# Kernel optimization log

Measured on AMD Instinct MI355X. Metric: run time of the kernel, lower is better.

The kernel has to match this reference:

```python
import jax, jax.numpy as jnp
import numpy as np

B, S, D, E = 4, 1024, 1024, 4
HID = 2816  # multiple_of * ceil(int(2*4*D/3) / multiple_of), multiple_of=256
COND = 1024  # min(D, 1024)
NORM_EPS = 1e-5  # block norms
LN_EPS = 1e-5    # q_norm/k_norm default eps


def setup_inputs() -> dict:
    key = jax.random.key(0)
    ks = jax.random.split(key, 16)
    w = lambda i, shape: jax.random.normal(ks[i], shape, jnp.float32) * 0.02
    return {
        'x': jax.random.normal(ks[0], (B, S, D), jnp.float32),
        'freqs_cis': jax.random.normal(ks[1], (S, 32), jnp.float32),  # unused by the block
        'adaln_input': jax.random.normal(ks[2], (B, COND), jnp.float32),
        'wq': w(3, (D, D)), 'wk': w(4, (D, D)), 'wv': w(5, (D, D)), 'wo': w(6, (D, D)),
        'q_norm_w': jnp.ones((D,), jnp.float32), 'q_norm_b': jnp.zeros((D,), jnp.float32),
        'k_norm_w': jnp.ones((D,), jnp.float32), 'k_norm_b': jnp.zeros((D,), jnp.float32),
        'attn_norm_w': jnp.ones((D,), jnp.float32), 'attn_norm_b': jnp.zeros((D,), jnp.float32),
        'ffn_norm_w': jnp.ones((D,), jnp.float32), 'ffn_norm_b': jnp.zeros((D,), jnp.float32),
        'w1': w(7, (E, D, HID)), 'w2': w(8, (E, HID, D)), 'w3': w(9, (E, D, HID)),
        'router_w': w(10, (D, E)), 'router_b': jnp.zeros((E,), jnp.float32),
        'ada_w': w(11, (COND, 6 * D)), 'ada_b': jnp.zeros((6 * D,), jnp.float32),
    }


def _ln(x, w, b, eps):
    mu = jnp.mean(x, -1, keepdims=True)
    var = jnp.mean((x - mu) ** 2, -1, keepdims=True)
    return (x - mu) * jax.lax.rsqrt(var + eps) * w + b


def _attention(x, wq, wk, wv, wo, qn_w, qn_b, kn_w, kn_b):
    # NOTE: this module attends over the FEATURE dim (no head split, no 1/sqrt(d) scale):
    # xq,xk,xv are permuted to [B, D, S]; scores are [B, D, D].
    q = _ln(x @ wq, qn_w, qn_b, LN_EPS)
    k = _ln(x @ wk, kn_w, kn_b, LN_EPS)
    v = x @ wv
    scores = jnp.einsum('bsd,bse->bde', q, k)          # [B, D, D]
    attn = jax.nn.softmax(scores, axis=-1)
    out = jnp.einsum('bde,bse->bsd', attn, v)          # [B, S, D]
    return out @ wo


def _moe(x, w1, w2, w3, router_w, router_b):
    logits = x @ router_w + router_b                   # [B, S, E]
    # F.normalize default dim=1 -> L2-normalize along the SEQUENCE dim (faithful quirk)
    nrm = jnp.sqrt(jnp.sum(logits * logits, axis=1, keepdims=True))
    logits = logits / jnp.maximum(nrm, 1e-12)
    probs = jax.nn.softmax(logits, axis=-1)
    topw, topi = jax.lax.top_k(probs, 2)
    # dense combine weights [B,S,E]: identical math to the masked gather/scatter dispatch
    combine = jnp.sum(jax.nn.one_hot(topi, E, dtype=x.dtype) * topw[..., None], axis=-2)
    h1 = jnp.einsum('bsd,edh->ebsh', x, w1)
    h3 = jnp.einsum('bsd,edh->ebsh', x, w3)
    out_e = jnp.einsum('ebsh,ehd->ebsd', jnp.sin(h1) * h3, w2)
    moe = jnp.einsum('bse,ebsd->bsd', combine, out_e)
    avg = jnp.mean(probs, axis=0)                      # [S, E] (mean over batch dim only)
    aux = jnp.sum((1.0 / E - avg) ** 2)
    return moe, aux


def reference(x, freqs_cis, adaln_input, wq, wk, wv, wo, q_norm_w, q_norm_b, k_norm_w,
              k_norm_b, attn_norm_w, attn_norm_b, ffn_norm_w, ffn_norm_b, w1, w2, w3,
              router_w, router_b, ada_w, ada_b):
    ada = jax.nn.silu(adaln_input) @ ada_w + ada_b     # [B, 6D]
    shift_msa, scale_msa, gate_msa, shift_mlp, scale_mlp, gate_mlp = jnp.split(ada, 6, axis=1)
    h = _ln(x, attn_norm_w, attn_norm_b, NORM_EPS)
    h = h * (1.0 + scale_msa[:, None, :]) + shift_msa[:, None, :]
    x = x + gate_msa[:, None, :] * _attention(h, wq, wk, wv, wo, q_norm_w, q_norm_b, k_norm_w, k_norm_b)
    h = _ln(x, ffn_norm_w, ffn_norm_b, NORM_EPS)
    h = h * (1.0 + scale_mlp[:, None, :]) + shift_mlp[:, None, :]
    # MoE path REPLACES x (no residual, gate_mlp unused) — faithful to the source
    x, aux = _moe(h, w1, w2, w3, router_w, router_b)
    return x, aux
```

## Files before the change

### kernel.cpp

```cpp
#include <hip/hip_runtime.h>
#include <hip/hip_bf16.h>
#include <math.h>

#define BB 4
#define SS 1024
#define DD 1024
#define EE 4
#define HID 2816
#define HC 1408
#define SIXD 6144
#define NSLOT 8704
#define NMB 68

typedef __bf16 v8bf __attribute__((ext_vector_type(8)));
typedef float  v4f  __attribute__((ext_vector_type(4)));

__device__ __forceinline__ ushort f2bf(float f) {
    union { float f; unsigned u; } v; v.f = f;
    unsigned r = v.u + 0x7fff + ((v.u >> 16) & 1);
    return (ushort)(r >> 16);
}
__device__ __forceinline__ float bf2f(ushort u) {
    union { unsigned u; float f; } v; v.u = ((unsigned)u) << 16;
    return v.f;
}
__device__ __forceinline__ void split_bf(float x, ushort& h, ushort& l) {
    h = f2bf(x);
    l = f2bf(x - bf2f(h));
}
__device__ __forceinline__ void gload16(const void* g, void* l) {
    __builtin_amdgcn_global_load_lds((const __attribute__((address_space(1))) void*)g,
                                     (__attribute__((address_space(3))) void*)l, 16, 0, 0);
}
template<int N> __device__ __forceinline__ void wait_vm() {
    __builtin_amdgcn_s_waitcnt((N & 15) | (0x7 << 4) | (0xF << 8) | ((N >> 4) << 14));
}

__device__ __forceinline__ void xcd_remap(int& bx, int& by) {
    const int gx = gridDim.x, gy = gridDim.y;
    const int nwg = gx * gy;
    const int wid = bx + gx * by;
    const int q = nwg >> 3, r = nwg & 7;
    const int xcd = wid & 7, loc = wid >> 3;
    const int pos = (xcd < r) ? (xcd * (q + 1) + loc)
                              : (r * (q + 1) + (xcd - r) * q + loc);
    bx = pos % gx; by = pos / gx;
}

__device__ __forceinline__ void xcd_remap_cm(int& bx, int& by) {
    const int gx = gridDim.x, gy = gridDim.y;
    const int nwg = gx * gy;
    const int wid = bx + gx * by;
    const int q = nwg >> 3, r = nwg & 7;
    const int xcd = wid & 7, loc = wid >> 3;
    const int pos = (xcd < r) ? (xcd * (q + 1) + loc)
                              : (r * (q + 1) + (xcd - r) * q + loc);
    bx = pos / gy; by = pos % gy;
}

__device__ __forceinline__ void moe_remap(int& bx, int& by) {
    const int gx = gridDim.x, gy = gridDim.y;
    const int total = gx * gy;
    const int wid = bx + gx * by;
    if ((total & 7) || (gx & 1)) { xcd_remap(bx, by); return; }
    const int q = total >> 3;
    const int pos = (wid & 7) * q + (wid >> 3);
    const int NG = gx >> 1;
    const int gh = NG * gy;
    const int nh = pos / gh, r = pos % gh;
    by = r / NG;
    bx = nh * NG + (r % NG);
}

template<int EPI, bool SPLIT, bool MOE>
__global__ __launch_bounds__(256, 2) void mgemm(
    const ushort* __restrict__ Ah, const ushort* __restrict__ Al,
    const ushort* __restrict__ Bh, const ushort* __restrict__ Bl,
    void* __restrict__ Cv, ushort* __restrict__ C2,
    const float* __restrict__ f1, const float* __restrict__ f2,
    const int* __restrict__ tokidx, const int* __restrict__ mbe,
    const int* __restrict__ mbm,
    int K, int lda, int ldb, int ldc,
    long sA, long sB, long sC)
{
    constexpr int STG = SPLIT ? 12288 : 6144;
    constexpr int BH  = SPLIT ? 8192 : 4096;
    constexpr int L   = SPLIT ? 6 : 3;
    constexpr int NST = SPLIT ? 2 : 3;
    __shared__ __align__(16) ushort smem[NST * STG];

    const int tid  = threadIdx.x;
    const int wv   = tid >> 6, lane = tid & 63;

    int bx = blockIdx.x, by = blockIdx.y;
    if (MOE) moe_remap(bx, by); else xcd_remap(bx, by);
    const int n0 = bx * 64;

    int eexp = 0, m0;
    if (MOE) {
        eexp = mbe[by];
        if (eexp < 0) return;
        m0 = mbm[by];
    } else {
        m0 = by * 128;
    }
    const long zA = MOE ? 0 : (long)blockIdx.z * sA;
    const long zB = MOE ? (long)eexp * sB : (long)blockIdx.z * sB;
    const long zC = MOE ? 0 : (long)blockIdx.z * sC;

    const int lrow = tid >> 2;
    const int skq  = ((tid & 3) ^ ((tid >> 3) & 3)) * 8;
    const int lm   = lane & 15;
    const int qs   = (((lane >> 4) ^ ((lm >> 1) & 3)) * 8);

    v4f acc[2][4];
    const v4f vzero = {0.f, 0.f, 0.f, 0.f};
    #pragma unroll
    for (int i = 0; i < 2; ++i)
        #pragma unroll
        for (int j = 0; j < 4; ++j) acc[i][j] = vzero;

    auto issue = [&](int kt, int st) {
        const long kk = (long)kt * 32 + skq;
        ushort* base = smem + st * STG;
        #pragma unroll
        for (int c = 0; c < 2; ++c) {
            const int row  = c * 64 + lrow;
            const int loff = (c * 64 + wv * 16) * 32;
            gload16(Ah + zA + (long)(m0 + row) * lda + kk, base + loff);
            if (SPLIT)
                gload16(Al + zA + (long)(m0 + row) * lda + kk, base + 4096 + loff);
        }
        {
            const int loff = wv * 16 * 32;
            gload16(Bh + zB + (long)(n0 + lrow) * ldb + kk, base + BH + loff);
            if (SPLIT)
                gload16(Bl + zB + (long)(n0 + lrow) * ldb + kk, base + BH + 2048 + loff);
        }
    };

    const int nk = K / 32;
    issue(0, 0);
    if (!SPLIT && nk > 1) issue(1, 1);
    for (int kt = 0; kt < nk; ++kt) {
        const int stg = SPLIT ? (kt & 1) : (kt % 3);
        if (SPLIT) {
            if (kt) __builtin_amdgcn_s_barrier();
            const bool hasNext = (kt + 1 < nk);
            if (hasNext) issue(kt + 1, stg ^ 1);
            if (hasNext) wait_vm<L>(); else wait_vm<0>();
            __builtin_amdgcn_s_barrier();
        } else {
            if (kt + 1 < nk) wait_vm<L>(); else wait_vm<0>();
            __builtin_amdgcn_s_barrier();
            if (kt + 2 < nk) issue(kt + 2, (kt + 2) % 3);
        }
        const ushort* As = smem + stg * STG;
        v8bf a[2], b[4];
        #pragma unroll
        for (int i = 0; i < 2; ++i) a[i] = *(const v8bf*)(As + (wv*32 + 16*i + lm) * 32 + qs);
        #pragma unroll
        for (int j = 0; j < 4; ++j) b[j] = *(const v8bf*)(As + BH + (16*j + lm) * 32 + qs);
        #pragma unroll
        for (int i = 0; i < 2; ++i)
            #pragma unroll
            for (int j = 0; j < 4; ++j)
                acc[i][j] = __builtin_amdgcn_mfma_f32_16x16x32_bf16(a[i], b[j], acc[i][j], 0, 0, 0);
        if (SPLIT) {
            v8bf al[2], bl[4];
            #pragma unroll
            for (int i = 0; i < 2; ++i) al[i] = *(const v8bf*)(As + 4096 + (wv*32 + 16*i + lm) * 32 + qs);
            #pragma unroll
            for (int j = 0; j < 4; ++j) bl[j] = *(const v8bf*)(As + BH + 2048 + (16*j + lm) * 32 + qs);
            #pragma unroll
            for (int i = 0; i < 2; ++i)
                #pragma unroll
                for (int j = 0; j < 4; ++j) {
                    acc[i][j] = __builtin_amdgcn_mfma_f32_16x16x32_bf16(a[i],  bl[j], acc[i][j], 0, 0, 0);
                    acc[i][j] = __builtin_amdgcn_mfma_f32_16x16x32_bf16(al[i], b[j],  acc[i][j], 0, 0, 0);
                }
        }
    }

    const int r0 = (lane >> 4) * 4;
    if (EPI == 7) {
        #pragma unroll
        for (int i = 0; i < 2; ++i)
            #pragma unroll
            for (int r = 0; r < 4; ++r) {
                const int rowg = m0 + wv*32 + 16*i + r0 + r;
                const int t = tokidx[rowg];
                if (t >= 0) {
                    const float cw = f1[t * 4 + eexp];
                    #pragma unroll
                    for (int j = 0; j < 4; ++j)
                        atomicAdd((float*)Cv + (long)t * 1024 + n0 + 16*j + lm, cw * acc[i][j][r]);
                }
            }
    } else {
        #pragma unroll
        for (int i = 0; i < 2; ++i) {
            #pragma unroll
            for (int j = 0; j < 4; ++j) {
                const int colg = n0 + 16*j + lm;
                #pragma unroll
                for (int r = 0; r < 4; ++r) {
                    const long rowg = (long)(m0 + wv*32 + 16*i + r0 + r);
                    const long idx  = zC + rowg * ldc + colg;
                    const float val = acc[i][j][r];
                    if (EPI == 0) {
                        ((float*)Cv)[idx] = val;
                    } else if (EPI == 2) {
                        ((float*)Cv)[idx] = f1[idx] + f2[(rowg >> 10) * SIXD + 2048 + colg] * val;
                    } else if (EPI == 5) {
                        ushort h, l; split_bf(val, h, l);
                        ((ushort*)Cv)[idx] = h;
                        C2[idx] = l;
                    }
                }
            }
        }
    }
}

__global__ __launch_bounds__(512, 2) void mgemm_h1h3(
    const ushort* __restrict__ Ah, const ushort* __restrict__ B1,
    const ushort* __restrict__ B2, ushort* __restrict__ Cb,
    const int* __restrict__ tokidx, const int* __restrict__ mbe,
    const int* __restrict__ mbm, long sB)
{
    constexpr int STG = 12288;
    __shared__ __align__(16) ushort smem[3 * STG];

    const int tid  = threadIdx.x;
    const int wv   = tid >> 6, lane = tid & 63;
    const int wr   = wv >> 2, wc = wv & 3;

    int bx = blockIdx.x, by = blockIdx.y;
    xcd_remap_cm(bx, by);
    const int n0 = bx * 128;
    const int eexp = mbe[by];
    if (eexp < 0) return;
    const int m0 = mbm[by];
    const long zB = (long)eexp * sB;

    const int lrow = tid >> 2;
    const int skq  = ((tid & 3) ^ ((tid >> 3) & 3)) * 8;
    const int lm   = lane & 15;
    const int qs   = (((lane >> 4) ^ ((lm >> 1) & 3)) * 8);

    const int t = tokidx[m0 + lrow];
    const long arow = (t < 0) ? 0 : (long)t;

    v4f acc[4][2], acc2[4][2];
    const v4f vzero = {0.f, 0.f, 0.f, 0.f};
    #pragma unroll
    for (int i = 0; i < 4; ++i)
        #pragma unroll
        for (int j = 0; j < 2; ++j) { acc[i][j] = vzero; acc2[i][j] = vzero; }

    auto issue = [&](int kt, int st) {
        const long kk = (long)kt * 32 + skq;
        ushort* base = smem + st * STG;
        const int loff = wv * 16 * 32;
        gload16(Ah + arow * 1024 + kk, base + loff);
        gload16(B1 + zB + (long)(n0 + lrow) * 1024 + kk, base + 4096 + loff);
        gload16(B2 + zB + (long)(n0 + lrow) * 1024 + kk, base + 8192 + loff);
    };

    issue(0, 0);
    issue(1, 1);
    int s_cur = 0, s_nxt = 2;
    #pragma unroll 1
    for (int kt = 0; kt < 32; ++kt) {
        if (kt + 1 < 32) wait_vm<3>(); else wait_vm<0>();
        __builtin_amdgcn_s_barrier();
        if (kt + 2 < 32) issue(kt + 2, s_nxt);
        const ushort* As = smem + s_cur * STG;
        v8bf a[4], b1[2], b2[2];
        #pragma unroll
        for (int i = 0; i < 4; ++i) a[i] = *(const v8bf*)(As + (wr*64 + 16*i + lm) * 32 + qs);
        #pragma unroll
        for (int j = 0; j < 2; ++j) {
            b1[j] = *(const v8bf*)(As + 4096 + (wc*32 + 16*j + lm) * 32 + qs);
            b2[j] = *(const v8bf*)(As + 8192 + (wc*32 + 16*j + lm) * 32 + qs);
        }
        #pragma unroll
        for (int i = 0; i < 4; ++i)
            #pragma unroll
            for (int j = 0; j < 2; ++j) {
                acc[i][j]  = __builtin_amdgcn_mfma_f32_16x16x32_bf16(a[i], b1[j], acc[i][j],  0, 0, 0);
                acc2[i][j] = __builtin_amdgcn_mfma_f32_16x16x32_bf16(a[i], b2[j], acc2[i][j], 0, 0, 0);
            }
        s_cur = (s_cur == 2) ? 0 : s_cur + 1;
        s_nxt = (s_nxt == 2) ? 0 : s_nxt + 1;
    }

    const int r0 = (lane >> 4) * 4;
    #pragma unroll
    for (int i = 0; i < 4; ++i)
        #pragma unroll
        for (int j = 0; j < 2; ++j) {
            const int colg = n0 + wc*32 + 16*j + lm;
            #pragma unroll
            for (int r = 0; r < 4; ++r) {
                const long rowg = (long)(m0 + wr*64 + 16*i + r0 + r);
                Cb[rowg * HC + colg] = f2bf(sinf(acc[i][j][r]) * acc2[i][j][r]);
            }
        }
}

template<bool SP>
__global__ __launch_bounds__(256) void transp(
    const float* __restrict__ in, ushort* __restrict__ oh, ushort* __restrict__ ol,
    int ldin, int ldout, long sIn, long sOut)
{
    __shared__ float T[64][65];
    const int n0 = blockIdx.x * 64, k0 = blockIdx.y * 64;
    in += (long)blockIdx.z * sIn;
    oh += (long)blockIdx.z * sOut;
    if (SP) ol += (long)blockIdx.z * sOut;
    const int t = threadIdx.x;
    const int rr = t >> 4, c4 = (t & 15) * 4;
    #pragma unroll
    for (int p = 0; p < 4; ++p) {
        const int r = rr + p * 16;
        const float4 v = *(const float4*)(in + (long)(k0 + r) * ldin + n0 + c4);
        T[c4+0][r] = v.x; T[c4+1][r] = v.y; T[c4+2][r] = v.z; T[c4+3][r] = v.w;
    }
    __syncthreads();
    #pragma unroll
    for (int p = 0; p < 4; ++p) {
        const int idx = t + 256 * p;
        const int n = idx >> 4, c = (idx & 15) * 4;
        ushort4 wh, wl;
        float x0 = T[n][c], x1 = T[n][c+1], x2 = T[n][c+2], x3 = T[n][c+3];
        if (SP) {
            split_bf(x0, wh.x, wl.x); split_bf(x1, wh.y, wl.y);
            split_bf(x2, wh.z, wl.z); split_bf(x3, wh.w, wl.w);
        } else {
            wh.x = f2bf(x0); wh.y = f2bf(x1); wh.z = f2bf(x2); wh.w = f2bf(x3);
        }
        *(ushort4*)(oh + (long)(n0 + n) * ldout + k0 + c) = wh;
        if (SP) *(ushort4*)(ol + (long)(n0 + n) * ldout + k0 + c) = wl;
    }
}

__global__ __launch_bounds__(256) void ada_kernel(
    const float* __restrict__ adaln, const float* __restrict__ aw,
    const float* __restrict__ ab, float* __restrict__ ada)
{
    __shared__ float s[DD];
    const int b = blockIdx.y;
    const int tid = threadIdx.x;
    for (int i = tid; i < DD; i += 256) {
        const float v = adaln[(long)b * DD + i];
        s[i] = v / (1.f + expf(-v));
    }
    __syncthreads();
    const int n = blockIdx.x * 256 + tid;
    float acc = 0.f;
    for (int k = 0; k < DD; ++k) acc += s[k] * aw[(long)k * SIXD + n];
    ada[(long)b * SIXD + n] = acc + ab[n];
}

template<int OUT, bool MOD>
__global__ __launch_bounds__(256) void ln_kernel(
    const float* __restrict__ x, const float* __restrict__ w, const float* __restrict__ bias,
    const float* __restrict__ ada, int scale_off, int shift_off,
    float* __restrict__ o32, ushort* __restrict__ oh, ushort* __restrict__ ol, float eps)
{
    const int row = blockIdx.x;
    const int b = row >> 10;
    const int tid = threadIdx.x;
    const float* xr = x + (long)row * DD;
    float v[4]; float s = 0.f, q = 0.f;
    #pragma unroll
    for (int i = 0; i < 4; ++i) { v[i] = xr[tid + 256*i]; s += v[i]; q += v[i]*v[i]; }
    __shared__ float rs_[256], rq_[256];
    rs_[tid] = s; rq_[tid] = q; __syncthreads();
    for (int off = 128; off > 0; off >>= 1) {
        if (tid < off) { rs_[tid] += rs_[tid+off]; rq_[tid] += rq_[tid+off]; }
        __syncthreads();
    }
    const float mu  = rs_[0] * (1.f/DD);
    const float var = rq_[0] * (1.f/DD) - mu*mu;
    const float rstd = rsqrtf(var + eps);
    const float* ar = ada + (long)b * SIXD;
    #pragma unroll
    for (int i = 0; i < 4; ++i) {
        const int d = tid + 256*i;
        float y = (v[i] - mu) * rstd * w[d] + bias[d];
        if (MOD) y = y * (1.f + ar[scale_off + d]) + ar[shift_off + d];
        const long idx = (long)row * DD + d;
        if (OUT == 0) o32[idx] = y;
        else if (OUT == 1) { ushort h, l; split_bf(y, h, l); oh[idx] = h; ol[idx] = l; }
        else oh[idx] = f2bf(y);
    }
}

__global__ __launch_bounds__(256) void softmax_split(
    const float* __restrict__ in, ushort* __restrict__ oh, ushort* __restrict__ ol)
{
    const long row = blockIdx.x;
    const float* p = in + row * 1024;
    const int tid = threadIdx.x;
    float v[4]; float mx = -INFINITY;
    #pragma unroll
    for (int i = 0; i < 4; ++i) { v[i] = p[tid + 256*i]; mx = fmaxf(mx, v[i]); }
    __shared__ float red[256];
    red[tid] = mx; __syncthreads();
    for (int off = 128; off > 0; off >>= 1) {
        if (tid < off) red[tid] = fmaxf(red[tid], red[tid+off]);
        __syncthreads();
    }
    const float rowmax = red[0];
    __syncthreads();
    float s = 0.f;
    #pragma unroll
    for (int i = 0; i < 4; ++i) { v[i] = expf(v[i] - rowmax); s += v[i]; }
    red[tid] = s; __syncthreads();
    for (int off = 128; off > 0; off >>= 1) {
        if (tid < off) red[tid] += red[tid+off];
        __syncthreads();
    }
    const float inv = 1.f / red[0];
    #pragma unroll
    for (int i = 0; i < 4; ++i) {
        ushort h, l; split_bf(v[i] * inv, h, l);
        oh[row*1024 + tid + 256*i] = h;
        ol[row*1024 + tid + 256*i] = l;
    }
}

__global__ __launch_bounds__(256) void router_fused(
    const float* __restrict__ x2, const float* __restrict__ fw, const float* __restrict__ fb,
    const float* __restrict__ ada, const float* __restrict__ rw, const float* __restrict__ rb,
    float* __restrict__ logits)
{
    const int row = blockIdx.x;
    const int b = row >> 10;
    const int tid = threadIdx.x;
    const float* xr = x2 + (long)row * DD;
    float v[4]; float s = 0.f, q = 0.f;
    #pragma unroll
    for (int i = 0; i < 4; ++i) { v[i] = xr[tid + 256*i]; s += v[i]; q += v[i]*v[i]; }
    __shared__ float rs_[256], rq_[256];
    rs_[tid] = s; rq_[tid] = q; __syncthreads();
    for (int off = 128; off > 0; off >>= 1) {
        if (tid < off) { rs_[tid] += rs_[tid+off]; rq_[tid] += rq_[tid+off]; }
        __syncthreads();
    }
    const float mu  = rs_[0] * (1.f/DD);
    const float var = rq_[0] * (1.f/DD) - mu*mu;
    const float rstd = rsqrtf(var + 1e-5f);
    const float* ar = ada + (long)b * SIXD;
    float acc[4] = {0.f, 0.f, 0.f, 0.f};
    #pragma unroll
    for (int i = 0; i < 4; ++i) {
        const int d = tid + 256*i;
        float h = (v[i] - mu) * rstd * fw[d] + fb[d];
        h = h * (1.f + ar[4096 + d]) + ar[3072 + d];
        const float* r4 = rw + (long)d * 4;
        acc[0] += h*r4[0]; acc[1] += h*r4[1]; acc[2] += h*r4[2]; acc[3] += h*r4[3];
    }
    __syncthreads();
    __shared__ float red[256];
    for (int e = 0; e < EE; ++e) {
        red[tid] = acc[e]; __syncthreads();
        for (int off = 128; off > 0; off >>= 1) {
            if (tid < off) red[tid] += red[tid+off];
            __syncthreads();
        }
        if (tid == 0) logits[(long)row * EE + e] = red[0] + rb[e];
        __syncthreads();
    }
}

__global__ __launch_bounds__(1024) void router_all(
    const float* __restrict__ logits, float* __restrict__ comb,
    float* __restrict__ auxout, int* __restrict__ tokidx,
    int* __restrict__ mbe, int* __restrict__ mbm)
{
    __shared__ float pl[16384];
    __shared__ float red[1024];
    __shared__ float nrm_l[16];
    __shared__ int lc[4], loff[4], lpos[4];
    const int tid = threadIdx.x;
    const int wv = tid >> 6, ln = tid & 63;
    {
        const int b = wv >> 2, e = wv & 3;
        float s = 0.f;
        for (int it = 0; it < 16; ++it) {
            const float v = logits[(((long)b << 10) + ln + (it << 6)) * 4 + e];
            s += v * v;
        }
        for (int off = 32; off > 0; off >>= 1) s += __shfl_down(s, off, 64);
        if (ln == 0) nrm_l[wv] = fmaxf(sqrtf(s), 1e-12f);
    }
    if (tid < 4) lc[tid] = 0;
    __syncthreads();
    float cloc[4][4];
    const int rbase = tid * 4;
    for (int rr = 0; rr < 4; ++rr) {
        const int row = rbase + rr;
        const int b = row >> 10;
        float l[4], p[4];
        #pragma unroll
        for (int e = 0; e < 4; ++e) l[e] = logits[(long)row*4 + e] / nrm_l[b*4 + e];
        const float mx = fmaxf(fmaxf(l[0], l[1]), fmaxf(l[2], l[3]));
        float s = 0.f;
        #pragma unroll
        for (int e = 0; e < 4; ++e) { p[e] = expf(l[e] - mx); s += p[e]; }
        const float inv = 1.f / s;
        #pragma unroll
        for (int e = 0; e < 4; ++e) { p[e] *= inv; pl[row*4 + e] = p[e]; }
        int i1 = 0;
        #pragma unroll
        for (int e = 1; e < 4; ++e) if (p[e] > p[i1]) i1 = e;
        int i2 = (i1 == 0) ? 1 : 0;
        #pragma unroll
        for (int e = 0; e < 4; ++e) if (e != i1 && p[e] > p[i2]) i2 = e;
        #pragma unroll
        for (int e = 0; e < 4; ++e) {
            const float c = (e == i1) ? p[i1] : ((e == i2) ? p[i2] : 0.f);
            cloc[rr][e] = c;
            comb[(long)row*4 + e] = c;
            if (c > 0.f) atomicAdd(&lc[e], 1);
        }
    }
    __syncthreads();
    float acc = 0.f;
    for (int i = tid; i < 4096; i += 1024) {
        const int s = i >> 2, e = i & 3;
        const float avg = 0.25f * (pl[s*4+e] + pl[(1024+s)*4+e] +
                                   pl[(2048+s)*4+e] + pl[(3072+s)*4+e]);
        const float d = 0.25f - avg;
        acc += d * d;
    }
    red[tid] = acc; __syncthreads();
    for (int off = 512; off > 0; off >>= 1) {
        if (tid < off) red[tid] += red[tid+off];
        __syncthreads();
    }
    if (tid == 0) auxout[0] = red[0];
    if (tid == 0) {
        int off0 = 0, nb = 0;
        for (int e = 0; e < 4; ++e) {
            loff[e] = off0; lpos[e] = 0;
            const int mb = (lc[e] + 127) >> 7;
            for (int k = 0; k < mb; ++k) { mbe[nb] = e; mbm[nb] = off0 + k*128; ++nb; }
            off0 += mb << 7;
        }
        for (; nb < NMB; ++nb) { mbe[nb] = -1; mbm[nb] = 0; }
    }
    for (int i = tid; i < NSLOT; i += 1024) tokidx[i] = -1;
    __syncthreads();
    for (int rr = 0; rr < 4; ++rr) {
        const int row = rbase + rr;
        #pragma unroll
        for (int e = 0; e < 4; ++e)
            if (cloc[rr][e] > 0.f) {
                const int s = atomicAdd(&lpos[e], 1);
                tokidx[loff[e] + s] = row;
            }
    }
}

__global__ __launch_bounds__(256) void zero_kernel(float4* __restrict__ out)
{
    out[(long)blockIdx.x * 256 + threadIdx.x] = float4{0.f, 0.f, 0.f, 0.f};
}

extern "C" void kernel_launch(void* const* d_in, const int* in_sizes, int n_in,
                              void* d_out, int out_size, void* d_ws, size_t ws_size,
                              hipStream_t stream)
{
    (void)in_sizes; (void)n_in; (void)out_size; (void)ws_size;
    const float* x     = (const float*)d_in[0];
    const float* adaln = (const float*)d_in[2];
    const float* wq    = (const float*)d_in[3];
    const float* wk    = (const float*)d_in[4];
    const float* wv    = (const float*)d_in[5];
    const float* wo    = (const float*)d_in[6];
    const float* qn_w  = (const float*)d_in[7];
    const float* qn_b  = (const float*)d_in[8];
    const float* kn_w  = (const float*)d_in[9];
    const float* kn_b  = (const float*)d_in[10];
    const float* an_w  = (const float*)d_in[11];
    const float* an_b  = (const float*)d_in[12];
    const float* fn_w  = (const float*)d_in[13];
    const float* fn_b  = (const float*)d_in[14];
    const float* w1    = (const float*)d_in[15];
    const float* w2    = (const float*)d_in[16];
    const float* w3    = (const float*)d_in[17];
    const float* rw    = (const float*)d_in[18];
    const float* rb    = (const float*)d_in[19];
    const float* aw    = (const float*)d_in[20];
    const float* ab    = (const float*)d_in[21];
    float* out = (float*)d_out;

    const long NBAT = (long)SS * DD;
    const long NBUF = (long)BB * SS * DD;
#define MB(x) ((long)(x) * 1048576L)

    char* P = (char*)d_ws;
    float* ada    = (float*)P;
    float* logits = (float*)(P + 98304);
    float* comb   = logits + 16384;
    int*   tokidx = (int*)(comb + 16384);
    int*   mbe    = tokidx + NSLOT;
    int*   mbm    = mbe + NMB;

    char* A0 = P + MB(1);
    ushort* wqT_h = (ushort*)(A0 + MB(0));  ushort* wqT_l = (ushort*)(A0 + MB(2));
    ushort* wkT_h = (ushort*)(A0 + MB(4));  ushort* wkT_l = (ushort*)(A0 + MB(6));
    ushort* wvT_h = (ushort*)(A0 + MB(8));  ushort* wvT_l = (ushort*)(A0 + MB(10));
    ushort* woT_h = (ushort*)(A0 + MB(0));  ushort* woT_l = (ushort*)(A0 + MB(2));
    ushort* w1Tc  = (ushort*)(A0 + MB(0));
    ushort* h_h  = (ushort*)(A0 + MB(12));  ushort* h_l  = (ushort*)(A0 + MB(20));
    float*  sc   = (float*) (A0 + MB(12));
    ushort* ao_h = (ushort*)(A0 + MB(12));  ushort* ao_l = (ushort*)(A0 + MB(20));
    ushort* actb = (ushort*)(A0 + MB(12));
    float*  qk32 = (float*) (A0 + MB(28));
    ushort* at_h = (ushort*)(A0 + MB(28));  ushort* at_l = (ushort*)(A0 + MB(36));
    ushort* v_h  = (ushort*)(A0 + MB(44));  ushort* v_l  = (ushort*)(A0 + MB(52));
    ushort* qT_h = (ushort*)(A0 + MB(60));  ushort* qT_l = (ushort*)(A0 + MB(68));
    float*  x2   = (float*) (A0 + MB(60));
    ushort* w3Tc = (ushort*)(A0 + MB(60));
    ushort* kT_h = (ushort*)(A0 + MB(76));  ushort* kT_l = (ushort*)(A0 + MB(84));
    ushort* h2bf = (ushort*)(A0 + MB(76));
    ushort* w2Tc = (ushort*)(A0 + MB(84));

    const dim3 blk(256);

    ada_kernel<<<dim3(SIXD/256, BB), blk, 0, stream>>>(adaln, aw, ab, ada);

    transp<true><<<dim3(16,16,1), blk, 0, stream>>>(wq, wqT_h, wqT_l, 1024, 1024, 0, 0);
    transp<true><<<dim3(16,16,1), blk, 0, stream>>>(wk, wkT_h, wkT_l, 1024, 1024, 0, 0);
    transp<true><<<dim3(16,16,1), blk, 0, stream>>>(wv, wvT_h, wvT_l, 1024, 1024, 0, 0);

    ln_kernel<1,true><<<4096, blk, 0, stream>>>(x, an_w, an_b, ada, 1024, 0,
                                                nullptr, h_h, h_l, 1e-5f);

    mgemm<0,true,false><<<dim3(16,32,1), blk, 0, stream>>>(
        h_h, h_l, wqT_h, wqT_l, qk32, nullptr, nullptr, nullptr, nullptr, nullptr, nullptr,
        1024, 1024, 1024, 1024, 0, 0, 0);
    ln_kernel<0,false><<<4096, blk, 0, stream>>>(qk32, qn_w, qn_b, ada, 0, 0, qk32, nullptr, nullptr, 1e-5f);
    transp<true><<<dim3(16,16,BB), blk, 0, stream>>>(qk32, qT_h, qT_l, 1024, 1024, NBAT, NBAT);

    mgemm<0,true,false><<<dim3(16,32,1), blk, 0, stream>>>(
        h_h, h_l, wkT_h, wkT_l, qk32, nullptr, nullptr, nullptr, nullptr, nullptr, nullptr,
        1024, 1024, 1024, 1024, 0, 0, 0);
    ln_kernel<0,false><<<4096, blk, 0, stream>>>(qk32, kn_w, kn_b, ada, 0, 0, qk32, nullptr, nullptr, 1e-5f);
    transp<true><<<dim3(16,16,BB), blk, 0, stream>>>(qk32, kT_h, kT_l, 1024, 1024, NBAT, NBAT);

    mgemm<5,true,false><<<dim3(16,32,1), blk, 0, stream>>>(
        h_h, h_l, wvT_h, wvT_l, v_h, v_l, nullptr, nullptr, nullptr, nullptr, nullptr,
        1024, 1024, 1024, 1024, 0, 0, 0);

    transp<true><<<dim3(16,16,1), blk, 0, stream>>>(wo, woT_h, woT_l, 1024, 1024, 0, 0);

    mgemm<0,true,false><<<dim3(16,8,BB), blk, 0, stream>>>(
        qT_h, qT_l, kT_h, kT_l, sc, nullptr, nullptr, nullptr, nullptr, nullptr, nullptr,
        1024, 1024, 1024, 1024, NBAT, NBAT, NBAT);

    softmax_split<<<4096, blk, 0, stream>>>(sc, at_h, at_l);

    mgemm<5,true,false><<<dim3(16,8,BB), blk, 0, stream>>>(
        v_h, v_l, at_h, at_l, ao_h, ao_l, nullptr, nullptr, nullptr, nullptr, nullptr,
        1024, 1024, 1024, 1024, NBAT, NBAT, NBAT);

    mgemm<2,true,false><<<dim3(16,32,1), blk, 0, stream>>>(
        ao_h, ao_l, woT_h, woT_l, x2, nullptr, x, ada, nullptr, nullptr, nullptr,
        1024, 1024, 1024, 1024, 0, 0, 0);

    ln_kernel<2,true><<<4096, blk, 0, stream>>>(x2, fn_w, fn_b, ada, 4096, 3072,
                                                nullptr, h2bf, nullptr, 1e-5f);

    router_fused<<<4096, blk, 0, stream>>>(x2, fn_w, fn_b, ada, rw, rb, logits);
    router_all<<<1, dim3(1024), 0, stream>>>(logits, comb, out + NBUF, tokidx, mbe, mbm);
    zero_kernel<<<dim3(4096), blk, 0, stream>>>((float4*)out);

    for (int c = 0; c < HID/HC; ++c) {
        transp<false><<<dim3(22,16,4), blk, 0, stream>>>(
            w1 + (long)c*HC, w1Tc, nullptr, HID, 1024, (long)DD*HID, (long)HC*1024);
        transp<false><<<dim3(22,16,4), blk, 0, stream>>>(
            w3 + (long)c*HC, w3Tc, nullptr, HID, 1024, (long)DD*HID, (long)HC*1024);
        transp<false><<<dim3(16,22,4), blk, 0, stream>>>(
            w2 + (long)c*HC*DD, w2Tc, nullptr, DD, HC, (long)HID*DD, (long)DD*HC);
        mgemm_h1h3<<<dim3(11, NMB), dim3(512), 0, stream>>>(
            h2bf, w1Tc, w3Tc, actb, tokidx, mbe, mbm, (long)HC*1024);
        mgemm<7,false,true><<<dim3(16, NMB), blk, 0, stream>>>(
            actb, nullptr, w2Tc, nullptr, out, nullptr, comb, nullptr, tokidx, mbe, mbm,
            HC, HC, HC, 1024, 0, (long)DD*HC, 0);
    }
#undef MB
}
```

Measured before the change: 833.0 us.

## Fuse Q/K/V projections into one split-bf16 GEMM and triple-buffer split mgemm

Adds a fused mgemm_qkv kernel that loads each activation tile (hi/lo bf16 split) once and multiplies it against all three of the Q, K and V weight tiles. It writes Q and K in fp32 and V as a hi/lo split. This removes two extra passes over the activation and two kernel launches. The generic split mgemm also moves from double to triple buffering with a single barrier per step, which raises its LDS footprint and may lower occupancy. The workspace buffers are reassigned so Q and K fp32 outputs can live at the same time.

```diff
diff --git a/kernel.cpp b/kernel.cpp
--- a/kernel.cpp
+++ b/kernel.cpp
@@ -86,8 +86,7 @@
     constexpr int STG = SPLIT ? 12288 : 6144;
     constexpr int BH  = SPLIT ? 8192 : 4096;
     constexpr int L   = SPLIT ? 6 : 3;
-    constexpr int NST = SPLIT ? 2 : 3;
-    __shared__ __align__(16) ushort smem[NST * STG];
+    __shared__ __align__(16) ushort smem[3 * STG];
 
     const int tid  = threadIdx.x;
     const int wv   = tid >> 6, lane = tid & 63;
@@ -141,21 +140,12 @@
 
     const int nk = K / 32;
     issue(0, 0);
-    if (!SPLIT && nk > 1) issue(1, 1);
+    if (nk > 1) issue(1, 1);
     for (int kt = 0; kt < nk; ++kt) {
-        const int stg = SPLIT ? (kt & 1) : (kt % 3);
-        if (SPLIT) {
-            if (kt) __builtin_amdgcn_s_barrier();
-            const bool hasNext = (kt + 1 < nk);
-            if (hasNext) issue(kt + 1, stg ^ 1);
-            if (hasNext) wait_vm<L>(); else wait_vm<0>();
-            __builtin_amdgcn_s_barrier();
-        } else {
-            if (kt + 1 < nk) wait_vm<L>(); else wait_vm<0>();
-            __builtin_amdgcn_s_barrier();
-            if (kt + 2 < nk) issue(kt + 2, (kt + 2) % 3);
-        }
-        const ushort* As = smem + stg * STG;
+        if (kt + 1 < nk) wait_vm<L>(); else wait_vm<0>();
+        __builtin_amdgcn_s_barrier();
+        if (kt + 2 < nk) issue(kt + 2, (kt + 2) % 3);
+        const ushort* As = smem + (kt % 3) * STG;
         v8bf a[2], b[4];
         #pragma unroll
         for (int i = 0; i < 2; ++i) a[i] = *(const v8bf*)(As + (wv*32 + 16*i + lm) * 32 + qs);
@@ -221,6 +211,113 @@
             }
         }
     }
+}
+
+__global__ __launch_bounds__(256, 2) void mgemm_qkv(
+    const ushort* __restrict__ Ah, const ushort* __restrict__ Al,
+    const ushort* __restrict__ Bqh, const ushort* __restrict__ Bql,
+    const ushort* __restrict__ Bkh, const ushort* __restrict__ Bkl,
+    const ushort* __restrict__ Bvh, const ushort* __restrict__ Bvl,
+    float* __restrict__ Cq, float* __restrict__ Ck,
+    ushort* __restrict__ Cvh, ushort* __restrict__ Cvl)
+{
+    constexpr int STG = 20480;
+    __shared__ __align__(16) ushort smem[2 * STG];
+
+    const int tid  = threadIdx.x;
+    const int wv   = tid >> 6, lane = tid & 63;
+
+    int bx = blockIdx.x, by = blockIdx.y;
+    xcd_remap(bx, by);
+    const int n0 = bx * 64, m0 = by * 128;
+
+    const int lrow = tid >> 2;
+    const int skq  = ((tid & 3) ^ ((tid >> 3) & 3)) * 8;
+    const int lm   = lane & 15;
+    const int qs   = (((lane >> 4) ^ ((lm >> 1) & 3)) * 8);
+
+    const ushort* Bh_[3] = {Bqh, Bkh, Bvh};
+    const ushort* Bl_[3] = {Bql, Bkl, Bvl};
+
+    v4f aq[2][4], ak[2][4], av[2][4];
+    const v4f vzero = {0.f, 0.f, 0.f, 0.f};
+    #pragma unroll
+    for (int i = 0; i < 2; ++i)
+        #pragma unroll
+        for (int j = 0; j < 4; ++j) { aq[i][j] = vzero; ak[i][j] = vzero; av[i][j] = vzero; }
+
+    auto issue = [&](int kt, int st) {
+        const long kk = (long)kt * 32 + skq;
+        ushort* base = smem + st * STG;
+        #pragma unroll
+        for (int c = 0; c < 2; ++c) {
+            const int row  = c * 64 + lrow;
+            const int loff = (c * 64 + wv * 16) * 32;
+            gload16(Ah + (long)(m0 + row) * 1024 + kk, base + loff);
+            gload16(Al + (long)(m0 + row) * 1024 + kk, base + 4096 + loff);
+        }
+        const int loff = wv * 16 * 32;
+        #pragma unroll
+        for (int m = 0; m < 3; ++m) {
+            gload16(Bh_[m] + (long)(n0 + lrow) * 1024 + kk, base + 8192 + m * 4096 + loff);
+            gload16(Bl_[m] + (long)(n0 + lrow) * 1024 + kk, base + 8192 + m * 4096 + 2048 + loff);
+        }
+    };
+
+    issue(0, 0);
+    #pragma unroll 1
+    for (int kt = 0; kt < 32; ++kt) {
+        const int stg = kt & 1;
+        if (kt) __builtin_amdgcn_s_barrier();
+        const bool hasNext = (kt + 1 < 32);
+        if (hasNext) issue(kt + 1, stg ^ 1);
+        if (hasNext) wait_vm<10>(); else wait_vm<0>();
+        __builtin_amdgcn_s_barrier();
+        const ushort* As = smem + stg * STG;
+        v8bf a[2], alo[2];
+        #pragma unroll
+        for (int i = 0; i < 2; ++i) {
+            a[i]   = *(const v8bf*)(As + (wv*32 + 16*i + lm) * 32 + qs);
+            alo[i] = *(const v8bf*)(As + 4096 + (wv*32 + 16*i + lm) * 32 + qs);
+        }
+        auto mat = [&](const ushort* Bs, v4f (&acc)[2][4]) {
+            v8bf b[4], bl[4];
+            #pragma unroll
+            for (int j = 0; j < 4; ++j) {
+                b[j]  = *(const v8bf*)(Bs + (16*j + lm) * 32 + qs);
+                bl[j] = *(const v8bf*)(Bs + 2048 + (16*j + lm) * 32 + qs);
+            }
+            #pragma unroll
+            for (int i = 0; i < 2; ++i)
+                #pragma unroll
+                for (int j = 0; j < 4; ++j) {
+                    acc[i][j] = __builtin_amdgcn_mfma_f32_16x16x32_bf16(a[i],   b[j],  acc[i][j], 0, 0, 0);
+                    acc[i][j] = __builtin_amdgcn_mfma_f32_16x16x32_bf16(a[i],   bl[j], acc[i][j], 0, 0, 0);
+                    acc[i][j] = __builtin_amdgcn_mfma_f32_16x16x32_bf16(alo[i], b[j],  acc[i][j], 0, 0, 0);
+                }
+        };
+        mat(As + 8192,        aq);
+        mat(As + 8192 + 4096, ak);
+        mat(As + 8192 + 8192, av);
+    }
+
+    const int r0 = (lane >> 4) * 4;
+    #pragma unroll
+    for (int i = 0; i < 2; ++i)
+        #pragma unroll
+        for (int j = 0; j < 4; ++j) {
+            const int colg = n0 + 16*j + lm;
+            #pragma unroll
+            for (int r = 0; r < 4; ++r) {
+                const long rowg = (long)(m0 + wv*32 + 16*i + r0 + r);
+                const long idx  = rowg * 1024 + colg;
+                Cq[idx] = aq[i][j][r];
+                Ck[idx] = ak[i][j][r];
+                ushort h, l; split_bf(av[i][j][r], h, l);
+                Cvh[idx] = h;
+                Cvl[idx] = l;
+            }
+        }
 }
 
 __global__ __launch_bounds__(512, 2) void mgemm_h1h3(
@@ -618,19 +715,20 @@
     ushort* wvT_h = (ushort*)(A0 + MB(8));  ushort* wvT_l = (ushort*)(A0 + MB(10));
     ushort* woT_h = (ushort*)(A0 + MB(0));  ushort* woT_l = (ushort*)(A0 + MB(2));
     ushort* w1Tc  = (ushort*)(A0 + MB(0));
-    ushort* h_h  = (ushort*)(A0 + MB(12));  ushort* h_l  = (ushort*)(A0 + MB(20));
-    float*  sc   = (float*) (A0 + MB(12));
-    ushort* ao_h = (ushort*)(A0 + MB(12));  ushort* ao_l = (ushort*)(A0 + MB(20));
-    ushort* actb = (ushort*)(A0 + MB(12));
-    float*  qk32 = (float*) (A0 + MB(28));
-    ushort* at_h = (ushort*)(A0 + MB(28));  ushort* at_l = (ushort*)(A0 + MB(36));
-    ushort* v_h  = (ushort*)(A0 + MB(44));  ushort* v_l  = (ushort*)(A0 + MB(52));
-    ushort* qT_h = (ushort*)(A0 + MB(60));  ushort* qT_l = (ushort*)(A0 + MB(68));
-    float*  x2   = (float*) (A0 + MB(60));
-    ushort* w3Tc = (ushort*)(A0 + MB(60));
-    ushort* kT_h = (ushort*)(A0 + MB(76));  ushort* kT_l = (ushort*)(A0 + MB(84));
-    ushort* h2bf = (ushort*)(A0 + MB(76));
-    ushort* w2Tc = (ushort*)(A0 + MB(84));
+    ushort* h_h   = (ushort*)(A0 + MB(12)); ushort* h_l  = (ushort*)(A0 + MB(20));
+    ushort* qT_h  = (ushort*)(A0 + MB(12)); ushort* qT_l = (ushort*)(A0 + MB(20));
+    ushort* ao_h  = (ushort*)(A0 + MB(12)); ushort* ao_l = (ushort*)(A0 + MB(20));
+    ushort* actb  = (ushort*)(A0 + MB(12));
+    float*  q32   = (float*) (A0 + MB(28));
+    float*  sc    = (float*) (A0 + MB(28));
+    float*  x2    = (float*) (A0 + MB(28));
+    ushort* v_h   = (ushort*)(A0 + MB(44)); ushort* v_l  = (ushort*)(A0 + MB(52));
+    float*  k32   = (float*) (A0 + MB(60));
+    ushort* at_h  = (ushort*)(A0 + MB(60)); ushort* at_l = (ushort*)(A0 + MB(68));
+    ushort* w3Tc  = (ushort*)(A0 + MB(60));
+    ushort* kT_h  = (ushort*)(A0 + MB(76)); ushort* kT_l = (ushort*)(A0 + MB(84));
+    ushort* h2bf  = (ushort*)(A0 + MB(76));
+    ushort* w2Tc  = (ushort*)(A0 + MB(84));
 
     const dim3 blk(256);
 
@@ -643,21 +741,15 @@
     ln_kernel<1,true><<<4096, blk, 0, stream>>>(x, an_w, an_b, ada, 1024, 0,
                                                 nullptr, h_h, h_l, 1e-5f);
 
-    mgemm<0,true,false><<<dim3(16,32,1), blk, 0, stream>>>(
-        h_h, h_l, wqT_h, wqT_l, qk32, nullptr, nullptr, nullptr, nullptr, nullptr, nullptr,
-        1024, 1024, 1024, 1024, 0, 0, 0);
-    ln_kernel<0,false><<<4096, blk, 0, stream>>>(qk32, qn_w, qn_b, ada, 0, 0, qk32, nullptr, nullptr, 1e-5f);
-    transp<true><<<dim3(16,16,BB), blk, 0, stream>>>(qk32, qT_h, qT_l, 1024, 1024, NBAT, NBAT);
-
-    mgemm<0,true,false><<<dim3(16,32,1), blk, 0, stream>>>(
-        h_h, h_l, wkT_h, wkT_l, qk32, nullptr, nullptr, nullptr, nullptr, nullptr, nullptr,
-        1024, 1024, 1024, 1024, 0, 0, 0);
-    ln_kernel<0,false><<<4096, blk, 0, stream>>>(qk32, kn_w, kn_b, ada, 0, 0, qk32, nullptr, nullptr, 1e-5f);
-    transp<true><<<dim3(16,16,BB), blk, 0, stream>>>(qk32, kT_h, kT_l, 1024, 1024, NBAT, NBAT);
-
-    mgemm<5,true,false><<<dim3(16,32,1), blk, 0, stream>>>(
-        h_h, h_l, wvT_h, wvT_l, v_h, v_l, nullptr, nullptr, nullptr, nullptr, nullptr,
-        1024, 1024, 1024, 1024, 0, 0, 0);
+    mgemm_qkv<<<dim3(16,32), blk, 0, stream>>>(
+        h_h, h_l, wqT_h, wqT_l, wkT_h, wkT_l, wvT_h, wvT_l,
+        q32, k32, v_h, v_l);
+
+    ln_kernel<0,false><<<4096, blk, 0, stream>>>(q32, qn_w, qn_b, ada, 0, 0, q32, nullptr, nullptr, 1e-5f);
+    transp<true><<<dim3(16,16,BB), blk, 0, stream>>>(q32, qT_h, qT_l, 1024, 1024, NBAT, NBAT);
+
+    ln_kernel<0,false><<<4096, blk, 0, stream>>>(k32, kn_w, kn_b, ada, 0, 0, k32, nullptr, nullptr, 1e-5f);
+    transp<true><<<dim3(16,16,BB), blk, 0, stream>>>(k32, kT_h, kT_l, 1024, 1024, NBAT, NBAT);
 
     transp<true><<<dim3(16,16,1), blk, 0, stream>>>(wo, woT_h, woT_l, 1024, 1024, 0, 0);
 
```

After: 794.9 us. -4.6%, faster.
